# Kernel optimization log

Measured on AMD Instinct MI355X. Metric: run time of the kernel, lower is better.

The kernel has to match this reference:

```python
import jax, jax.numpy as jnp
import numpy as np

N, E, G = 50000, 800000, 64
D, DE, DIN, L = 64, 4, 11, 2


def _lin(x, w, b):
    return x @ w + b


def _bn(x, g, b, eps=1e-5):
    # BatchNorm1d in training mode: biased batch statistics over dim 0
    m = x.mean(0)
    v = x.var(0)
    return (x - m) * jax.lax.rsqrt(v + eps) * g + b


def setup_inputs() -> dict:
    key = jax.random.key(0)
    ks = iter(jax.random.split(key, 64))

    def rn(shape, s=0.05):
        return jax.random.normal(next(ks), shape, jnp.float32) * s

    inp = dict(
        x=rn((N, DIN), 1.0),
        pos=rn((N, 3), 1.0),
        edge_attr=rn((E, DE), 1.0),
        edge_index=jax.random.randint(next(ks), (2, E), 0, N),
        batch=jnp.sort(jax.random.randint(next(ks), (N,), 0, G)),
        lin_in_w=rn((DIN, D)), lin_in_b=jnp.zeros((D,), jnp.float32),
        lin_pred_w=rn((D, 1)), lin_pred_b=jnp.zeros((1,), jnp.float32),
        # per-layer stacked params (leading dim L)
        msg_w1=rn((L, 2 * D + DE + 1, D)), msg_b1=jnp.zeros((L, D), jnp.float32),
        msg_g1=jnp.ones((L, D), jnp.float32), msg_be1=jnp.zeros((L, D), jnp.float32),
        msg_w2=rn((L, D, D)), msg_b2=jnp.zeros((L, D), jnp.float32),
        msg_g2=jnp.ones((L, D), jnp.float32), msg_be2=jnp.zeros((L, D), jnp.float32),
        pos_w1=rn((L, D, D)), pos_b1=jnp.zeros((L, D), jnp.float32),
        pos_g=jnp.ones((L, D), jnp.float32), pos_be=jnp.zeros((L, D), jnp.float32),
        pos_w2=rn((L, D, 1)), pos_b2=jnp.zeros((L, 1), jnp.float32),
        upd_w1=rn((L, 2 * D, D)), upd_b1=jnp.zeros((L, D), jnp.float32),
        upd_g1=jnp.ones((L, D), jnp.float32), upd_be1=jnp.zeros((L, D), jnp.float32),
        upd_w2=rn((L, D, D)), upd_b2=jnp.zeros((L, D), jnp.float32),
        upd_g2=jnp.ones((L, D), jnp.float32), upd_be2=jnp.zeros((L, D), jnp.float32),
    )
    return inp


def reference(x, pos, edge_attr, edge_index, batch,
              lin_in_w, lin_in_b, lin_pred_w, lin_pred_b,
              msg_w1, msg_b1, msg_g1, msg_be1, msg_w2, msg_b2, msg_g2, msg_be2,
              pos_w1, pos_b1, pos_g, pos_be, pos_w2, pos_b2,
              upd_w1, upd_b1, upd_g1, upd_be1, upd_w2, upd_b2, upd_g2, upd_be2):
    src, dst = edge_index[0], edge_index[1]  # h_j = h[src], h_i = h[dst]
    h = x @ lin_in_w + lin_in_b
    p = pos
    deg = jnp.maximum(jax.ops.segment_sum(jnp.ones((E,), h.dtype), dst, N), 1.0)
    for l in range(L):
        h_i, h_j = h[dst], h[src]          # (E, D) gathers
        pd = p[dst] - p[src]               # (E, 3)
        radial = jnp.sum(pd * pd, axis=1, keepdims=True)  # (E, 1)
        m = jnp.concatenate([h_i, h_j, radial, edge_attr], -1)  # (E, 2D+DE+1)
        m = jax.nn.relu(_bn(_lin(m, msg_w1[l], msg_b1[l]), msg_g1[l], msg_be1[l]))
        m = jax.nn.relu(_bn(_lin(m, msg_w2[l], msg_b2[l]), msg_g2[l], msg_be2[l]))
        s = jax.nn.relu(_bn(_lin(m, pos_w1[l], pos_b1[l]), pos_g[l], pos_be[l]))
        s = _lin(s, pos_w2[l], pos_b2[l])  # (E, 1) scalar gate
        pos_upd = pd * s                   # (E, 3)
        m_aggr = jax.ops.segment_sum(m, dst, N)                    # sum aggr
        p_aggr = jax.ops.segment_sum(pos_upd, dst, N) / deg[:, None]  # mean aggr
        u = jnp.concatenate([h, m_aggr], -1)
        u = jax.nn.relu(_bn(_lin(u, upd_w1[l], upd_b1[l]), upd_g1[l], upd_be1[l]))
        u = jax.nn.relu(_bn(_lin(u, upd_w2[l], upd_b2[l]), upd_g2[l], upd_be2[l]))
        h = h + u          # residual on node features (MPNNModel style)
        p = p + p_aggr     # position update from layer
    cnt = jnp.maximum(jax.ops.segment_sum(jnp.ones((N,), h.dtype), batch, G), 1.0)
    h_graph = jax.ops.segment_sum(h, batch, G) / cnt[:, None]  # global_mean_pool
    out = h_graph @ lin_pred_w + lin_pred_b
    return out.reshape(-1)
```

## Files before the change

kernel.cpp:

```cpp
#include <hip/hip_runtime.h>

#define Nn 50000
#define Ee 800000
#define Gg 64
#define Dd 64
#define KIN 133
#define ES 68
#define EPS 1e-5f


__global__ __launch_bounds__(256) void k_lin_in(const float* __restrict__ x,
    const float* __restrict__ W, const float* __restrict__ B, float* __restrict__ h)
{
    __shared__ float Ws[11 * 64];
    __shared__ float Bs[64];
    int t = threadIdx.x;
    for (int i = t; i < 11 * 64; i += 256) Ws[i] = W[i];
    if (t < 64) Bs[t] = B[t];
    __syncthreads();
    int i = blockIdx.x * 256 + t;
    if (i < Nn * 64) {
        int n = i >> 6, c = i & 63;
        float acc = Bs[c];
        #pragma unroll
        for (int k = 0; k < 11; k++) acc += x[n * 11 + k] * Ws[k * 64 + c];
        h[i] = acc;
    }
}

__global__ __launch_bounds__(256) void k_deg(const int* __restrict__ ei, float* __restrict__ deg)
{
    int e = blockIdx.x * 256 + threadIdx.x;
    if (e < Ee) atomicAdd(&deg[ei[Ee + e]], 1.f);
}

__global__ __launch_bounds__(256) void k_cnt(const int* __restrict__ batch, float* __restrict__ cnt)
{
    int n = blockIdx.x * 256 + threadIdx.x;
    if (n < Nn) atomicAdd(&cnt[batch[n]], 1.f);
}


__global__ __launch_bounds__(256) void k_edge_lin1(
    const float* __restrict__ h, const float* __restrict__ p,
    const float* __restrict__ ea, const int* __restrict__ ei,
    const float* __restrict__ W, const float* __restrict__ B,
    float* __restrict__ ybuf, float* __restrict__ stats_out)
{
    __shared__ float Ws[KIN * 64];
    __shared__ float Bs[64];
    __shared__ float in_t[KIN * ES];
    int t = threadIdx.x;
    for (int i = t; i < KIN * 64; i += 256) Ws[i] = W[i];
    if (t < 64) Bs[t] = B[t];
    int tx = t & 15, ty = t >> 4;
    int c = t & 63, eg = t >> 6;
    float ssum[4] = {0, 0, 0, 0}, ssq[4] = {0, 0, 0, 0};
    for (int tile = blockIdx.x; tile < Ee / 64; tile += gridDim.x) {
        int te = tile * 64;
        __syncthreads();
        for (int e = eg; e < 64; e += 4) {
            int sr = ei[te + e], ds = ei[Ee + te + e];
            in_t[c * ES + e]        = h[(size_t)ds * 64 + c];
            in_t[(64 + c) * ES + e] = h[(size_t)sr * 64 + c];
        }
        if (t < 64) {
            int e = t;
            int sr = ei[te + e], ds = ei[Ee + te + e];
            float dx = p[ds * 3 + 0] - p[sr * 3 + 0];
            float dy = p[ds * 3 + 1] - p[sr * 3 + 1];
            float dz = p[ds * 3 + 2] - p[sr * 3 + 2];
            in_t[128 * ES + e] = dx * dx + dy * dy + dz * dz;
            float4 a4 = *(const float4*)&ea[(size_t)(te + e) * 4];
            in_t[129 * ES + e] = a4.x;
            in_t[130 * ES + e] = a4.y;
            in_t[131 * ES + e] = a4.z;
            in_t[132 * ES + e] = a4.w;
        }
        __syncthreads();
        float acc[4][4];
        #pragma unroll
        for (int i = 0; i < 4; i++)
            #pragma unroll
            for (int j = 0; j < 4; j++) acc[i][j] = Bs[4 * ty + j];
        for (int k = 0; k < KIN; k++) {
            float av[4], wv[4];
            *(float4*)av = *(const float4*)&in_t[k * ES + 4 * tx];
            *(float4*)wv = *(const float4*)&Ws[k * 64 + 4 * ty];
            #pragma unroll
            for (int i = 0; i < 4; i++)
                #pragma unroll
                for (int j = 0; j < 4; j++)
                    acc[i][j] += av[i] * wv[j];
        }
        #pragma unroll
        for (int i = 0; i < 4; i++) {
            size_t e = (size_t)te + 4 * tx + i;
            float4 o; o.x = acc[i][0]; o.y = acc[i][1]; o.z = acc[i][2]; o.w = acc[i][3];
            *(float4*)&ybuf[e * 64 + 4 * ty] = o;
            #pragma unroll
            for (int j = 0; j < 4; j++) { ssum[j] += acc[i][j]; ssq[j] += acc[i][j] * acc[i][j]; }
        }
    }
    #pragma unroll
    for (int j = 0; j < 4; j++) {
        float s = ssum[j], q = ssq[j];
        #pragma unroll
        for (int o2 = 1; o2 < 16; o2 <<= 1) { s += __shfl_xor(s, o2); q += __shfl_xor(q, o2); }
        if (tx == 0) {
            atomicAdd(&stats_out[4 * ty + j], s);
            atomicAdd(&stats_out[64 + 4 * ty + j], q);
        }
    }
}


template<int AGGR>
__global__ __launch_bounds__(256) void k_edge_lin64(
    const float* __restrict__ stats_in, const float* __restrict__ gg,
    const float* __restrict__ be,
    const float* __restrict__ W, const float* __restrict__ B,
    const int* __restrict__ ei, float* __restrict__ magg,
    float* __restrict__ ybuf, float* __restrict__ stats_out)
{
    __shared__ float Ws[64 * 64];
    __shared__ float As[64], Cs[64], Bs[64];
    __shared__ float in_t[64 * ES];
    int t = threadIdx.x;
    if (t < 64) {
        float mean = stats_in[t] * (1.f / Ee);
        float var  = stats_in[64 + t] * (1.f / Ee) - mean * mean;
        float a = gg[t] * rsqrtf(var + EPS);
        As[t] = a; Cs[t] = be[t] - mean * a; Bs[t] = B[t];
    }
    for (int i = t; i < 64 * 64; i += 256) Ws[i] = W[i];
    int tx = t & 15, ty = t >> 4;
    int c = t & 63, eg = t >> 6;
    float ssum[4] = {0, 0, 0, 0}, ssq[4] = {0, 0, 0, 0};
    for (int tile = blockIdx.x; tile < Ee / 64; tile += gridDim.x) {
        int te = tile * 64;
        __syncthreads();
        for (int e = eg; e < 64; e += 4) {
            float y = ybuf[(size_t)(te + e) * 64 + c];
            in_t[c * ES + e] = fmaxf(As[c] * y + Cs[c], 0.f);
        }
        __syncthreads();
        float acc[4][4];
        #pragma unroll
        for (int i = 0; i < 4; i++)
            #pragma unroll
            for (int j = 0; j < 4; j++) acc[i][j] = Bs[4 * ty + j];
        for (int k = 0; k < 64; k++) {
            float av[4], wv[4];
            *(float4*)av = *(const float4*)&in_t[k * ES + 4 * tx];
            *(float4*)wv = *(const float4*)&Ws[k * 64 + 4 * ty];
            #pragma unroll
            for (int i = 0; i < 4; i++)
                #pragma unroll
                for (int j = 0; j < 4; j++)
                    acc[i][j] += av[i] * wv[j];
        }
        if (AGGR) {
            for (int e = eg; e < 64; e += 4) {
                int ds = ei[Ee + te + e];
                atomicAdd(&magg[(size_t)ds * 64 + c], in_t[c * ES + e]);
            }
        }
        #pragma unroll
        for (int i = 0; i < 4; i++) {
            size_t e = (size_t)te + 4 * tx + i;
            float4 o; o.x = acc[i][0]; o.y = acc[i][1]; o.z = acc[i][2]; o.w = acc[i][3];
            *(float4*)&ybuf[e * 64 + 4 * ty] = o;
            #pragma unroll
            for (int j = 0; j < 4; j++) { ssum[j] += acc[i][j]; ssq[j] += acc[i][j] * acc[i][j]; }
        }
    }
    #pragma unroll
    for (int j = 0; j < 4; j++) {
        float s = ssum[j], q = ssq[j];
        #pragma unroll
        for (int o2 = 1; o2 < 16; o2 <<= 1) { s += __shfl_xor(s, o2); q += __shfl_xor(q, o2); }
        if (tx == 0) {
            atomicAdd(&stats_out[4 * ty + j], s);
            atomicAdd(&stats_out[64 + 4 * ty + j], q);
        }
    }
}


__global__ __launch_bounds__(256) void k_pos2(
    const float* __restrict__ stats_in, const float* __restrict__ gg, const float* __restrict__ be,
    const float* __restrict__ W2, const float* __restrict__ B2,
    const float* __restrict__ p, const int* __restrict__ ei,
    const float* __restrict__ ybuf, float* __restrict__ pagg)
{
    __shared__ float As[64], Cs[64], Ws[64];
    int t = threadIdx.x;
    if (t < 64) {
        float mean = stats_in[t] * (1.f / Ee);
        float var  = stats_in[64 + t] * (1.f / Ee) - mean * mean;
        float a = gg[t] * rsqrtf(var + EPS);
        As[t] = a; Cs[t] = be[t] - mean * a; Ws[t] = W2[t];
    }
    __syncthreads();
    int e = blockIdx.x * 256 + t;
    if (e >= Ee) return;
    float acc = B2[0];
    const float* row = &ybuf[(size_t)e * 64];
    #pragma unroll
    for (int u = 0; u < 16; u++) {
        float4 y = *(const float4*)&row[4 * u];
        acc += fmaxf(As[4 * u + 0] * y.x + Cs[4 * u + 0], 0.f) * Ws[4 * u + 0]
             + fmaxf(As[4 * u + 1] * y.y + Cs[4 * u + 1], 0.f) * Ws[4 * u + 1]
             + fmaxf(As[4 * u + 2] * y.z + Cs[4 * u + 2], 0.f) * Ws[4 * u + 2]
             + fmaxf(As[4 * u + 3] * y.w + Cs[4 * u + 3], 0.f) * Ws[4 * u + 3];
    }
    int sr = ei[e], ds = ei[Ee + e];
    float dx = p[ds * 3 + 0] - p[sr * 3 + 0];
    float dy = p[ds * 3 + 1] - p[sr * 3 + 1];
    float dz = p[ds * 3 + 2] - p[sr * 3 + 2];
    atomicAdd(&pagg[ds * 3 + 0], dx * acc);
    atomicAdd(&pagg[ds * 3 + 1], dy * acc);
    atomicAdd(&pagg[ds * 3 + 2], dz * acc);
}


__global__ __launch_bounds__(256) void k_node_lin1(
    const float* __restrict__ h, const float* __restrict__ magg,
    const float* __restrict__ W, const float* __restrict__ B,
    float* __restrict__ yn, float* __restrict__ stats_out)
{
    __shared__ float Ws[128 * 64];
    __shared__ float Bs[64];
    __shared__ float in_t[128 * ES];
    int t = threadIdx.x;
    for (int i = t; i < 128 * 64; i += 256) Ws[i] = W[i];
    if (t < 64) Bs[t] = B[t];
    int tx = t & 15, ty = t >> 4, c = t & 63, eg = t >> 6;
    float ssum[4] = {0, 0, 0, 0}, ssq[4] = {0, 0, 0, 0};
    int nT = (Nn + 63) / 64;
    for (int tile = blockIdx.x; tile < nT; tile += gridDim.x) {
        int te = tile * 64;
        __syncthreads();
        for (int e = eg; e < 64; e += 4) {
            int n = te + e;
            bool v = n < Nn;
            in_t[c * ES + e]        = v ? h[(size_t)n * 64 + c]    : 0.f;
            in_t[(64 + c) * ES + e] = v ? magg[(size_t)n * 64 + c] : 0.f;
        }
        __syncthreads();
        float acc[4][4];
        #pragma unroll
        for (int i = 0; i < 4; i++)
            #pragma unroll
            for (int j = 0; j < 4; j++) acc[i][j] = Bs[4 * ty + j];
        for (int k = 0; k < 128; k++) {
            float av[4], wv[4];
            *(float4*)av = *(const float4*)&in_t[k * ES + 4 * tx];
            *(float4*)wv = *(const float4*)&Ws[k * 64 + 4 * ty];
            #pragma unroll
            for (int i = 0; i < 4; i++)
                #pragma unroll
                for (int j = 0; j < 4; j++)
                    acc[i][j] += av[i] * wv[j];
        }
        #pragma unroll
        for (int i = 0; i < 4; i++) {
            int n = te + 4 * tx + i;
            if (n < Nn) {
                float4 o; o.x = acc[i][0]; o.y = acc[i][1]; o.z = acc[i][2]; o.w = acc[i][3];
                *(float4*)&yn[(size_t)n * 64 + 4 * ty] = o;
                #pragma unroll
                for (int j = 0; j < 4; j++) { ssum[j] += acc[i][j]; ssq[j] += acc[i][j] * acc[i][j]; }
            }
        }
    }
    #pragma unroll
    for (int j = 0; j < 4; j++) {
        float s = ssum[j], q = ssq[j];
        #pragma unroll
        for (int o2 = 1; o2 < 16; o2 <<= 1) { s += __shfl_xor(s, o2); q += __shfl_xor(q, o2); }
        if (tx == 0) {
            atomicAdd(&stats_out[4 * ty + j], s);
            atomicAdd(&stats_out[64 + 4 * ty + j], q);
        }
    }
}


__global__ __launch_bounds__(256) void k_node_lin64(
    const float* __restrict__ stats_in, const float* __restrict__ gg, const float* __restrict__ be,
    const float* __restrict__ W, const float* __restrict__ B,
    float* __restrict__ yn, float* __restrict__ stats_out)
{
    __shared__ float Ws[64 * 64];
    __shared__ float As[64], Cs[64], Bs[64];
    __shared__ float in_t[64 * ES];
    int t = threadIdx.x;
    if (t < 64) {
        float mean = stats_in[t] * (1.f / Nn);
        float var  = stats_in[64 + t] * (1.f / Nn) - mean * mean;
        float a = gg[t] * rsqrtf(var + EPS);
        As[t] = a; Cs[t] = be[t] - mean * a; Bs[t] = B[t];
    }
    for (int i = t; i < 64 * 64; i += 256) Ws[i] = W[i];
    int tx = t & 15, ty = t >> 4, c = t & 63, eg = t >> 6;
    float ssum[4] = {0, 0, 0, 0}, ssq[4] = {0, 0, 0, 0};
    int nT = (Nn + 63) / 64;
    for (int tile = blockIdx.x; tile < nT; tile += gridDim.x) {
        int te = tile * 64;
        __syncthreads();
        for (int e = eg; e < 64; e += 4) {
            int n = te + e;
            float y = (n < Nn) ? yn[(size_t)n * 64 + c] : 0.f;
            in_t[c * ES + e] = fmaxf(As[c] * y + Cs[c], 0.f);
        }
        __syncthreads();
        float acc[4][4];
        #pragma unroll
        for (int i = 0; i < 4; i++)
            #pragma unroll
            for (int j = 0; j < 4; j++) acc[i][j] = Bs[4 * ty + j];
        for (int k = 0; k < 64; k++) {
            float av[4], wv[4];
            *(float4*)av = *(const float4*)&in_t[k * ES + 4 * tx];
            *(float4*)wv = *(const float4*)&Ws[k * 64 + 4 * ty];
            #pragma unroll
            for (int i = 0; i < 4; i++)
                #pragma unroll
                for (int j = 0; j < 4; j++)
                    acc[i][j] += av[i] * wv[j];
        }
        #pragma unroll
        for (int i = 0; i < 4; i++) {
            int n = te + 4 * tx + i;
            if (n < Nn) {
                float4 o; o.x = acc[i][0]; o.y = acc[i][1]; o.z = acc[i][2]; o.w = acc[i][3];
                *(float4*)&yn[(size_t)n * 64 + 4 * ty] = o;
                #pragma unroll
                for (int j = 0; j < 4; j++) { ssum[j] += acc[i][j]; ssq[j] += acc[i][j] * acc[i][j]; }
            }
        }
    }
    #pragma unroll
    for (int j = 0; j < 4; j++) {
        float s = ssum[j], q = ssq[j];
        #pragma unroll
        for (int o2 = 1; o2 < 16; o2 <<= 1) { s += __shfl_xor(s, o2); q += __shfl_xor(q, o2); }
        if (tx == 0) {
            atomicAdd(&stats_out[4 * ty + j], s);
            atomicAdd(&stats_out[64 + 4 * ty + j], q);
        }
    }
}


__global__ __launch_bounds__(256) void k_node_update(
    const float* __restrict__ stats_in, const float* __restrict__ gg, const float* __restrict__ be,
    const float* __restrict__ yn, float* __restrict__ h,
    const float* __restrict__ p_in, float* __restrict__ p_out,
    const float* __restrict__ pagg, const float* __restrict__ deg)
{
    int i = blockIdx.x * 256 + threadIdx.x;
    if (i < Nn * 64) {
        int c = i & 63;
        float mean = stats_in[c] * (1.f / Nn);
        float var  = stats_in[64 + c] * (1.f / Nn) - mean * mean;
        float a = gg[c] * rsqrtf(var + EPS);
        float cc = be[c] - mean * a;
        h[i] += fmaxf(a * yn[i] + cc, 0.f);
    }
    if (i < Nn * 3) {
        float dg = fmaxf(deg[i / 3], 1.f);
        p_out[i] = p_in[i] + pagg[i] / dg;
    }
}


__global__ __launch_bounds__(256) void k_pool(const int* __restrict__ batch,
    const float* __restrict__ h, float* __restrict__ pool)
{
    int i = blockIdx.x * 256 + threadIdx.x;
    if (i < Nn * 64) {
        int n = i >> 6, c = i & 63;
        atomicAdd(&pool[(size_t)batch[n] * 64 + c], h[i]);
    }
}

__global__ void k_out(const float* __restrict__ pool, const float* __restrict__ cnt,
    const float* __restrict__ W, const float* __restrict__ B, float* __restrict__ out)
{
    int g = threadIdx.x;
    if (g < 64) {
        float acc = 0.f;
        for (int c = 0; c < 64; c++) acc += pool[g * 64 + c] * W[c];
        out[g] = acc / fmaxf(cnt[g], 1.f) + B[0];
    }
}


extern "C" void kernel_launch(void* const* d_in, const int* in_sizes, int n_in,
                              void* d_out, int out_size, void* d_ws, size_t ws_size,
                              hipStream_t stream)
{
    const float* x        = (const float*)d_in[0];
    const float* pos      = (const float*)d_in[1];
    const float* ea       = (const float*)d_in[2];
    const int*   ei       = (const int*)  d_in[3];
    const int*   batch    = (const int*)  d_in[4];
    const float* lin_in_w = (const float*)d_in[5];
    const float* lin_in_b = (const float*)d_in[6];
    const float* lin_pr_w = (const float*)d_in[7];
    const float* lin_pr_b = (const float*)d_in[8];
    const float* msg_w1   = (const float*)d_in[9];
    const float* msg_b1   = (const float*)d_in[10];
    const float* msg_g1   = (const float*)d_in[11];
    const float* msg_be1  = (const float*)d_in[12];
    const float* msg_w2   = (const float*)d_in[13];
    const float* msg_b2   = (const float*)d_in[14];
    const float* msg_g2   = (const float*)d_in[15];
    const float* msg_be2  = (const float*)d_in[16];
    const float* pos_w1   = (const float*)d_in[17];
    const float* pos_b1   = (const float*)d_in[18];
    const float* pos_g    = (const float*)d_in[19];
    const float* pos_be   = (const float*)d_in[20];
    const float* pos_w2   = (const float*)d_in[21];
    const float* pos_b2   = (const float*)d_in[22];
    const float* upd_w1   = (const float*)d_in[23];
    const float* upd_b1   = (const float*)d_in[24];
    const float* upd_g1   = (const float*)d_in[25];
    const float* upd_be1  = (const float*)d_in[26];
    const float* upd_w2   = (const float*)d_in[27];
    const float* upd_b2   = (const float*)d_in[28];
    const float* upd_g2   = (const float*)d_in[29];
    const float* upd_be2  = (const float*)d_in[30];
    float* out = (float*)d_out;

    float* ws = (float*)d_ws;
    size_t o = 0;
    float* h    = ws + o; o += (size_t)Nn * 64;
    float* ybuf = ws + o; o += (size_t)Ee * 64;
    float* yn   = ws + o; o += (size_t)Nn * 64;
    float* magg = ws + o; o += (size_t)Nn * 64;
    float* pagg = ws + o; o += (size_t)Nn * 3;
    float* pws  = ws + o; o += (size_t)Nn * 3;
    float* stats= ws + o; o += 1280;
    float* pool = ws + o; o += 64 * 64;
    float* cnt  = ws + o; o += 64;
    float* deg  = ws + o; o += Nn;
    if (ws_size < o * sizeof(float)) return;

    hipMemsetAsync(stats, 0, (size_t)(1280 + 64 * 64 + 64 + Nn) * sizeof(float), stream);
    k_lin_in<<<(Nn * 64 + 255) / 256, 256, 0, stream>>>(x, lin_in_w, lin_in_b, h);
    k_deg<<<(Ee + 255) / 256, 256, 0, stream>>>(ei, deg);
    k_cnt<<<(Nn + 255) / 256, 256, 0, stream>>>(batch, cnt);

    for (int l = 0; l < 2; l++) {
        hipMemsetAsync(magg, 0, ((size_t)Nn * 64 + (size_t)Nn * 3) * sizeof(float), stream);
        const float* pc = (l == 0) ? pos : pws;
        float* st = stats + (size_t)l * 5 * 128;
        k_edge_lin1<<<512, 256, 0, stream>>>(h, pc, ea, ei,
            msg_w1 + (size_t)l * KIN * 64, msg_b1 + l * 64, ybuf, st + 0 * 128);
        k_edge_lin64<0><<<1024, 256, 0, stream>>>(st + 0 * 128, msg_g1 + l * 64, msg_be1 + l * 64,
            msg_w2 + (size_t)l * 64 * 64, msg_b2 + l * 64, ei, nullptr, ybuf, st + 1 * 128);
        k_edge_lin64<1><<<1024, 256, 0, stream>>>(st + 1 * 128, msg_g2 + l * 64, msg_be2 + l * 64,
            pos_w1 + (size_t)l * 64 * 64, pos_b1 + l * 64, ei, magg, ybuf, st + 2 * 128);
        k_pos2<<<(Ee + 255) / 256, 256, 0, stream>>>(st + 2 * 128, pos_g + l * 64, pos_be + l * 64,
            pos_w2 + l * 64, pos_b2 + l, pc, ei, ybuf, pagg);
        k_node_lin1<<<782, 256, 0, stream>>>(h, magg,
            upd_w1 + (size_t)l * 128 * 64, upd_b1 + l * 64, yn, st + 3 * 128);
        k_node_lin64<<<782, 256, 0, stream>>>(st + 3 * 128, upd_g1 + l * 64, upd_be1 + l * 64,
            upd_w2 + (size_t)l * 64 * 64, upd_b2 + l * 64, yn, st + 4 * 128);
        k_node_update<<<(Nn * 64 + 255) / 256, 256, 0, stream>>>(st + 4 * 128,
            upd_g2 + l * 64, upd_be2 + l * 64, yn, h, pc, pws, pagg, deg);
    }
    k_pool<<<(Nn * 64 + 255) / 256, 256, 0, stream>>>(batch, h, pool);
    k_out<<<1, 64, 0, stream>>>(pool, cnt, lin_pr_w, lin_pr_b, out);
}
```

Baseline: 2.497 ms.

## Store edge activations feature-major and double-buffer edge tiles via direct global-to-LDS loads

The edge activation buffer switches from edge-major to feature-major layout, so each feature column over the edges is contiguous. The edge MLP kernels now stage tiles into double-buffered LDS with global_load_lds, prefetching the next tile during compute. BatchNorm+ReLU is folded into the GEMM inner loop, and the first edge kernel prefetches gathered node features in registers. This aims to hide gather and load latency and to coalesce loads in the pos2 kernel, at the cost of more LDS use, a new atomic pattern in the aggregation, and async-load ordering that relies on the existing barriers.

```diff
diff --git a/kernel.cpp b/kernel.cpp
--- a/kernel.cpp
+++ b/kernel.cpp
@@ -3,10 +3,23 @@
 #define Nn 50000
 #define Ee 800000
 #define Gg 64
-#define Dd 64
 #define KIN 133
 #define ES 68
 #define EPS 1e-5f
+
+#define AS1 __attribute__((address_space(1)))
+#define AS3 __attribute__((address_space(3)))
+
+__device__ __forceinline__ void load_lds16(const float* g, float* s) {
+    __builtin_amdgcn_global_load_lds((const AS1 void*)g, (AS3 void*)s, 16, 0, 0);
+}
+
+__device__ __forceinline__ void stage_lin(const float* __restrict__ g0, float* l0,
+                                          int t, int nfloats) {
+    int l = t & 63, w = t >> 6;
+    for (int ch = w; ch * 256 < nfloats; ch += 4)
+        load_lds16(g0 + ch * 256 + l * 4, l0 + ch * 256);
+}
 
 
 __global__ __launch_bounds__(256) void k_lin_in(const float* __restrict__ x,
@@ -45,7 +58,7 @@
     const float* __restrict__ h, const float* __restrict__ p,
     const float* __restrict__ ea, const int* __restrict__ ei,
     const float* __restrict__ W, const float* __restrict__ B,
-    float* __restrict__ ybuf, float* __restrict__ stats_out)
+    float* __restrict__ ybT, float* __restrict__ stats_out)
 {
     __shared__ float Ws[KIN * 64];
     __shared__ float Bs[64];
@@ -54,35 +67,82 @@
     for (int i = t; i < KIN * 64; i += 256) Ws[i] = W[i];
     if (t < 64) Bs[t] = B[t];
     int tx = t & 15, ty = t >> 4;
-    int c = t & 63, eg = t >> 6;
+    int cg = t & 15, es = t >> 4;
     float ssum[4] = {0, 0, 0, 0}, ssq[4] = {0, 0, 0, 0};
-    for (int tile = blockIdx.x; tile < Ee / 64; tile += gridDim.x) {
+
+    float4 hi[4], hj[4], eav;
+    float rad = 0.f;
+    int nt = Ee / 64;
+    int tile = blockIdx.x;
+
+    {
         int te = tile * 64;
-        __syncthreads();
-        for (int e = eg; e < 64; e += 4) {
-            int sr = ei[te + e], ds = ei[Ee + te + e];
-            in_t[c * ES + e]        = h[(size_t)ds * 64 + c];
-            in_t[(64 + c) * ES + e] = h[(size_t)sr * 64 + c];
+        #pragma unroll
+        for (int i = 0; i < 4; i++) {
+            int e = te + es * 4 + i;
+            int sr = ei[e], ds = ei[Ee + e];
+            hi[i] = *(const float4*)&h[(size_t)ds * 64 + 4 * cg];
+            hj[i] = *(const float4*)&h[(size_t)sr * 64 + 4 * cg];
         }
         if (t < 64) {
-            int e = t;
-            int sr = ei[te + e], ds = ei[Ee + te + e];
+            int e = te + t;
+            int sr = ei[e], ds = ei[Ee + e];
             float dx = p[ds * 3 + 0] - p[sr * 3 + 0];
             float dy = p[ds * 3 + 1] - p[sr * 3 + 1];
             float dz = p[ds * 3 + 2] - p[sr * 3 + 2];
-            in_t[128 * ES + e] = dx * dx + dy * dy + dz * dz;
-            float4 a4 = *(const float4*)&ea[(size_t)(te + e) * 4];
-            in_t[129 * ES + e] = a4.x;
-            in_t[130 * ES + e] = a4.y;
-            in_t[131 * ES + e] = a4.z;
-            in_t[132 * ES + e] = a4.w;
-        }
-        __syncthreads();
+            rad = dx * dx + dy * dy + dz * dz;
+            eav = *(const float4*)&ea[(size_t)e * 4];
+        }
+    }
+    {
+        #pragma unroll
+        for (int i = 0; i < 4; i++) {
+            float4 v, u;
+            v.x = ((const float*)&hi[0])[i]; v.y = ((const float*)&hi[1])[i];
+            v.z = ((const float*)&hi[2])[i]; v.w = ((const float*)&hi[3])[i];
+            u.x = ((const float*)&hj[0])[i]; u.y = ((const float*)&hj[1])[i];
+            u.z = ((const float*)&hj[2])[i]; u.w = ((const float*)&hj[3])[i];
+            *(float4*)&in_t[(4 * cg + i) * ES + es * 4] = v;
+            *(float4*)&in_t[(64 + 4 * cg + i) * ES + es * 4] = u;
+        }
+        if (t < 64) {
+            in_t[128 * ES + t] = rad;
+            in_t[129 * ES + t] = eav.x; in_t[130 * ES + t] = eav.y;
+            in_t[131 * ES + t] = eav.z; in_t[132 * ES + t] = eav.w;
+        }
+    }
+
+    for (; tile < nt; tile += gridDim.x) {
+        __syncthreads();
+        int nxt = tile + gridDim.x;
+        if (nxt < nt) {
+            int te = nxt * 64;
+            #pragma unroll
+            for (int i = 0; i < 4; i++) {
+                int e = te + es * 4 + i;
+                int sr = ei[e], ds = ei[Ee + e];
+                hi[i] = *(const float4*)&h[(size_t)ds * 64 + 4 * cg];
+                hj[i] = *(const float4*)&h[(size_t)sr * 64 + 4 * cg];
+            }
+            if (t < 64) {
+                int e = te + t;
+                int sr = ei[e], ds = ei[Ee + e];
+                float dx = p[ds * 3 + 0] - p[sr * 3 + 0];
+                float dy = p[ds * 3 + 1] - p[sr * 3 + 1];
+                float dz = p[ds * 3 + 2] - p[sr * 3 + 2];
+                rad = dx * dx + dy * dy + dz * dz;
+                eav = *(const float4*)&ea[(size_t)e * 4];
+            }
+        }
         float acc[4][4];
-        #pragma unroll
-        for (int i = 0; i < 4; i++)
-            #pragma unroll
-            for (int j = 0; j < 4; j++) acc[i][j] = Bs[4 * ty + j];
+        {
+            float4 b4 = *(const float4*)&Bs[4 * ty];
+            #pragma unroll
+            for (int i = 0; i < 4; i++) {
+                acc[i][0] = b4.x; acc[i][1] = b4.y; acc[i][2] = b4.z; acc[i][3] = b4.w;
+            }
+        }
+        #pragma unroll 7
         for (int k = 0; k < KIN; k++) {
             float av[4], wv[4];
             *(float4*)av = *(const float4*)&in_t[k * ES + 4 * tx];
@@ -93,13 +153,31 @@
                 for (int j = 0; j < 4; j++)
                     acc[i][j] += av[i] * wv[j];
         }
-        #pragma unroll
-        for (int i = 0; i < 4; i++) {
-            size_t e = (size_t)te + 4 * tx + i;
-            float4 o; o.x = acc[i][0]; o.y = acc[i][1]; o.z = acc[i][2]; o.w = acc[i][3];
-            *(float4*)&ybuf[e * 64 + 4 * ty] = o;
-            #pragma unroll
-            for (int j = 0; j < 4; j++) { ssum[j] += acc[i][j]; ssq[j] += acc[i][j] * acc[i][j]; }
+        int te = tile * 64;
+        #pragma unroll
+        for (int j = 0; j < 4; j++) {
+            float4 o; o.x = acc[0][j]; o.y = acc[1][j]; o.z = acc[2][j]; o.w = acc[3][j];
+            *(float4*)&ybT[(size_t)(4 * ty + j) * Ee + te + 4 * tx] = o;
+            ssum[j] += o.x + o.y + o.z + o.w;
+            ssq[j]  += o.x * o.x + o.y * o.y + o.z * o.z + o.w * o.w;
+        }
+        __syncthreads();
+        if (nxt < nt) {
+            #pragma unroll
+            for (int i = 0; i < 4; i++) {
+                float4 v, u;
+                v.x = ((const float*)&hi[0])[i]; v.y = ((const float*)&hi[1])[i];
+                v.z = ((const float*)&hi[2])[i]; v.w = ((const float*)&hi[3])[i];
+                u.x = ((const float*)&hj[0])[i]; u.y = ((const float*)&hj[1])[i];
+                u.z = ((const float*)&hj[2])[i]; u.w = ((const float*)&hj[3])[i];
+                *(float4*)&in_t[(4 * cg + i) * ES + es * 4] = v;
+                *(float4*)&in_t[(64 + 4 * cg + i) * ES + es * 4] = u;
+            }
+            if (t < 64) {
+                in_t[128 * ES + t] = rad;
+                in_t[129 * ES + t] = eav.x; in_t[130 * ES + t] = eav.y;
+                in_t[131 * ES + t] = eav.z; in_t[132 * ES + t] = eav.w;
+            }
         }
     }
     #pragma unroll
@@ -121,59 +199,92 @@
     const float* __restrict__ be,
     const float* __restrict__ W, const float* __restrict__ B,
     const int* __restrict__ ei, float* __restrict__ magg,
-    float* __restrict__ ybuf, float* __restrict__ stats_out)
+    float* __restrict__ ybT, float* __restrict__ stats_out)
 {
     __shared__ float Ws[64 * 64];
-    __shared__ float As[64], Cs[64], Bs[64];
-    __shared__ float in_t[64 * ES];
+    __shared__ float in_t[2 * 64 * 64];
+    __shared__ float ACs[128];
+    __shared__ float Bs[64];
     int t = threadIdx.x;
+    int l = t & 63, w = t >> 6;
+    int lr = l >> 4, lc = (l & 15) * 4;
+
+    stage_lin(W, Ws, t, 64 * 64);
     if (t < 64) {
         float mean = stats_in[t] * (1.f / Ee);
         float var  = stats_in[64 + t] * (1.f / Ee) - mean * mean;
         float a = gg[t] * rsqrtf(var + EPS);
-        As[t] = a; Cs[t] = be[t] - mean * a; Bs[t] = B[t];
-    }
-    for (int i = t; i < 64 * 64; i += 256) Ws[i] = W[i];
+        ACs[2 * t] = a; ACs[2 * t + 1] = be[t] - mean * a; Bs[t] = B[t];
+    }
+    int nt = Ee / 64;
+    int tile = blockIdx.x;
+    {
+        int te = tile * 64;
+        #pragma unroll
+        for (int q = 0; q < 4; q++) {
+            int ch = w * 4 + q;
+            load_lds16(ybT + (size_t)(ch * 4 + lr) * Ee + te + lc, in_t + ch * 256);
+        }
+    }
     int tx = t & 15, ty = t >> 4;
-    int c = t & 63, eg = t >> 6;
+    int cur = 0;
     float ssum[4] = {0, 0, 0, 0}, ssq[4] = {0, 0, 0, 0};
-    for (int tile = blockIdx.x; tile < Ee / 64; tile += gridDim.x) {
-        int te = tile * 64;
-        __syncthreads();
-        for (int e = eg; e < 64; e += 4) {
-            float y = ybuf[(size_t)(te + e) * 64 + c];
-            in_t[c * ES + e] = fmaxf(As[c] * y + Cs[c], 0.f);
-        }
-        __syncthreads();
+
+    for (; tile < nt; tile += gridDim.x) {
+        __syncthreads();
+        int nxt = tile + gridDim.x;
+        int dnode = 0;
+        if (AGGR) dnode = ei[Ee + tile * 64 + l];
+        if (nxt < nt) {
+            int te = nxt * 64;
+            float* dst = in_t + (cur ^ 1) * 4096;
+            #pragma unroll
+            for (int q = 0; q < 4; q++) {
+                int ch = w * 4 + q;
+                load_lds16(ybT + (size_t)(ch * 4 + lr) * Ee + te + lc, dst + ch * 256);
+            }
+        }
+        const float* buf = in_t + cur * 4096;
         float acc[4][4];
-        #pragma unroll
-        for (int i = 0; i < 4; i++)
-            #pragma unroll
-            for (int j = 0; j < 4; j++) acc[i][j] = Bs[4 * ty + j];
+        {
+            float4 b4 = *(const float4*)&Bs[4 * ty];
+            #pragma unroll
+            for (int i = 0; i < 4; i++) {
+                acc[i][0] = b4.x; acc[i][1] = b4.y; acc[i][2] = b4.z; acc[i][3] = b4.w;
+            }
+        }
+        #pragma unroll 8
         for (int k = 0; k < 64; k++) {
             float av[4], wv[4];
-            *(float4*)av = *(const float4*)&in_t[k * ES + 4 * tx];
+            *(float4*)av = *(const float4*)&buf[k * 64 + 4 * tx];
             *(float4*)wv = *(const float4*)&Ws[k * 64 + 4 * ty];
+            float a = ACs[2 * k], c = ACs[2 * k + 1];
+            float r[4];
+            #pragma unroll
+            for (int i = 0; i < 4; i++) r[i] = fmaxf(av[i] * a + c, 0.f);
             #pragma unroll
             for (int i = 0; i < 4; i++)
                 #pragma unroll
                 for (int j = 0; j < 4; j++)
-                    acc[i][j] += av[i] * wv[j];
+                    acc[i][j] += r[i] * wv[j];
         }
         if (AGGR) {
-            for (int e = eg; e < 64; e += 4) {
-                int ds = ei[Ee + te + e];
-                atomicAdd(&magg[(size_t)ds * 64 + c], in_t[c * ES + e]);
-            }
-        }
-        #pragma unroll
-        for (int i = 0; i < 4; i++) {
-            size_t e = (size_t)te + 4 * tx + i;
-            float4 o; o.x = acc[i][0]; o.y = acc[i][1]; o.z = acc[i][2]; o.w = acc[i][3];
-            *(float4*)&ybuf[e * 64 + 4 * ty] = o;
-            #pragma unroll
-            for (int j = 0; j < 4; j++) { ssum[j] += acc[i][j]; ssq[j] += acc[i][j] * acc[i][j]; }
-        }
+            #pragma unroll
+            for (int q = 0; q < 16; q++) {
+                int k = w * 16 + q;
+                float v = fmaxf(buf[k * 64 + l] * ACs[2 * k] + ACs[2 * k + 1], 0.f);
+                atomicAdd(&magg[(size_t)dnode * 64 + k], v);
+            }
+        }
+        int te = tile * 64;
+        #pragma unroll
+        for (int j = 0; j < 4; j++) {
+            float4 o; o.x = acc[0][j]; o.y = acc[1][j]; o.z = acc[2][j]; o.w = acc[3][j];
+            *(float4*)&ybT[(size_t)(4 * ty + j) * Ee + te + 4 * tx] = o;
+            ssum[j] += o.x + o.y + o.z + o.w;
+            ssq[j]  += o.x * o.x + o.y * o.y + o.z * o.z + o.w * o.w;
+        }
+        cur ^= 1;
     }
     #pragma unroll
     for (int j = 0; j < 4; j++) {
@@ -192,7 +303,7 @@
     const float* __restrict__ stats_in, const float* __restrict__ gg, const float* __restrict__ be,
     const float* __restrict__ W2, const float* __restrict__ B2,
     const float* __restrict__ p, const int* __restrict__ ei,
-    const float* __restrict__ ybuf, float* __restrict__ pagg)
+    const float* __restrict__ ybT, float* __restrict__ pagg)
 {
     __shared__ float As[64], Cs[64], Ws[64];
     int t = threadIdx.x;
@@ -204,17 +315,10 @@
     }
     __syncthreads();
     int e = blockIdx.x * 256 + t;
-    if (e >= Ee) return;
     float acc = B2[0];
-    const float* row = &ybuf[(size_t)e * 64];
-    #pragma unroll
-    for (int u = 0; u < 16; u++) {
-        float4 y = *(const float4*)&row[4 * u];
-        acc += fmaxf(As[4 * u + 0] * y.x + Cs[4 * u + 0], 0.f) * Ws[4 * u + 0]
-             + fmaxf(As[4 * u + 1] * y.y + Cs[4 * u + 1], 0.f) * Ws[4 * u + 1]
-             + fmaxf(As[4 * u + 2] * y.z + Cs[4 * u + 2], 0.f) * Ws[4 * u + 2]
-             + fmaxf(As[4 * u + 3] * y.w + Cs[4 * u + 3], 0.f) * Ws[4 * u + 3];
-    }
+    #pragma unroll 8
+    for (int k = 0; k < 64; k++)
+        acc += fmaxf(As[k] * ybT[(size_t)k * Ee + e] + Cs[k], 0.f) * Ws[k];
     int sr = ei[e], ds = ei[Ee + e];
     float dx = p[ds * 3 + 0] - p[sr * 3 + 0];
     float dy = p[ds * 3 + 1] - p[sr * 3 + 1];
@@ -439,7 +543,7 @@
     float* ws = (float*)d_ws;
     size_t o = 0;
     float* h    = ws + o; o += (size_t)Nn * 64;
-    float* ybuf = ws + o; o += (size_t)Ee * 64;
+    float* ybT  = ws + o; o += (size_t)Ee * 64;
     float* yn   = ws + o; o += (size_t)Nn * 64;
     float* magg = ws + o; o += (size_t)Nn * 64;
     float* pagg = ws + o; o += (size_t)Nn * 3;
@@ -460,13 +564,13 @@
         const float* pc = (l == 0) ? pos : pws;
         float* st = stats + (size_t)l * 5 * 128;
         k_edge_lin1<<<512, 256, 0, stream>>>(h, pc, ea, ei,
-            msg_w1 + (size_t)l * KIN * 64, msg_b1 + l * 64, ybuf, st + 0 * 128);
-        k_edge_lin64<0><<<1024, 256, 0, stream>>>(st + 0 * 128, msg_g1 + l * 64, msg_be1 + l * 64,
-            msg_w2 + (size_t)l * 64 * 64, msg_b2 + l * 64, ei, nullptr, ybuf, st + 1 * 128);
-        k_edge_lin64<1><<<1024, 256, 0, stream>>>(st + 1 * 128, msg_g2 + l * 64, msg_be2 + l * 64,
-            pos_w1 + (size_t)l * 64 * 64, pos_b1 + l * 64, ei, magg, ybuf, st + 2 * 128);
-        k_pos2<<<(Ee + 255) / 256, 256, 0, stream>>>(st + 2 * 128, pos_g + l * 64, pos_be + l * 64,
-            pos_w2 + l * 64, pos_b2 + l, pc, ei, ybuf, pagg);
+            msg_w1 + (size_t)l * KIN * 64, msg_b1 + l * 64, ybT, st + 0 * 128);
+        k_edge_lin64<0><<<768, 256, 0, stream>>>(st + 0 * 128, msg_g1 + l * 64, msg_be1 + l * 64,
+            msg_w2 + (size_t)l * 64 * 64, msg_b2 + l * 64, ei, nullptr, ybT, st + 1 * 128);
+        k_edge_lin64<1><<<768, 256, 0, stream>>>(st + 1 * 128, msg_g2 + l * 64, msg_be2 + l * 64,
+            pos_w1 + (size_t)l * 64 * 64, pos_b1 + l * 64, ei, magg, ybT, st + 2 * 128);
+        k_pos2<<<Ee / 256, 256, 0, stream>>>(st + 2 * 128, pos_g + l * 64, pos_be + l * 64,
+            pos_w2 + l * 64, pos_b2 + l, pc, ei, ybT, pagg);
         k_node_lin1<<<782, 256, 0, stream>>>(h, magg,
             upd_w1 + (size_t)l * 128 * 64, upd_b1 + l * 64, yn, st + 3 * 128);
         k_node_lin64<<<782, 256, 0, stream>>>(st + 3 * 128, upd_g1 + l * 64, upd_be1 + l * 64,
```

Measured after the change: 7.340 ms. +194.0%, slower.

## Swizzle edge buffers, async LDS loads with double buffering in edge MLP kernels

Applied to the files above, without the earlier changes.

Stores edge activations in an XOR-swizzled row-major layout so tiles can be copied straight into LDS with global_load_lds and read without bank conflicts. The 64-wide edge layers double-buffer the next tile's load behind the current tile's FMA loop and fold BN+ReLU into the operand read. The first edge layer now gathers node rows as float4 and uses k-chunked FMAs. This adds layout coupling across kernels (k_pos2 must unswizzle) and depends on async LDS load ordering being correctly synchronized.

```diff
diff --git a/kernel.cpp b/kernel.cpp
--- a/kernel.cpp
+++ b/kernel.cpp
@@ -2,11 +2,29 @@
 
 #define Nn 50000
 #define Ee 800000
-#define Gg 64
-#define Dd 64
 #define KIN 133
+#define SR 136
 #define ES 68
 #define EPS 1e-5f
+
+#define AS1 __attribute__((address_space(1)))
+#define AS3 __attribute__((address_space(3)))
+
+__device__ __forceinline__ void load_lds16(const float* g, float* s) {
+    __builtin_amdgcn_global_load_lds((const AS1 void*)g, (AS3 void*)s, 16, 0, 0);
+}
+
+#define BNRELU4(V, A4, C4) \
+    V.x = fmaxf(V.x * A4.x + C4.x, 0.f); \
+    V.y = fmaxf(V.y * A4.y + C4.y, 0.f); \
+    V.z = fmaxf(V.z * A4.z + C4.z, 0.f); \
+    V.w = fmaxf(V.w * A4.w + C4.w, 0.f);
+
+#define FMAROW(ACCI, AV) \
+    ACCI[0] += AV.x * w0.x; ACCI[0] += AV.y * w1.x; ACCI[0] += AV.z * w2.x; ACCI[0] += AV.w * w3.x; \
+    ACCI[1] += AV.x * w0.y; ACCI[1] += AV.y * w1.y; ACCI[1] += AV.z * w2.y; ACCI[1] += AV.w * w3.y; \
+    ACCI[2] += AV.x * w0.z; ACCI[2] += AV.y * w1.z; ACCI[2] += AV.z * w2.z; ACCI[2] += AV.w * w3.z; \
+    ACCI[3] += AV.x * w0.w; ACCI[3] += AV.y * w1.w; ACCI[3] += AV.z * w2.w; ACCI[3] += AV.w * w3.w;
 
 
 __global__ __launch_bounds__(256) void k_lin_in(const float* __restrict__ x,
@@ -47,22 +65,36 @@
     const float* __restrict__ W, const float* __restrict__ B,
     float* __restrict__ ybuf, float* __restrict__ stats_out)
 {
-    __shared__ float Ws[KIN * 64];
+    __shared__ float Ws[SR * 64];
     __shared__ float Bs[64];
-    __shared__ float in_t[KIN * ES];
+    __shared__ float in_t[64 * SR];
     int t = threadIdx.x;
-    for (int i = t; i < KIN * 64; i += 256) Ws[i] = W[i];
-    if (t < 64) Bs[t] = B[t];
+    {
+        int l = t & 63, w = t >> 6;
+        for (int ch = w; ch < 33; ch += 4)
+            load_lds16(W + ch * 256 + l * 4, Ws + ch * 256);
+    }
+    if (t < 64) { Ws[8448 + t] = W[8448 + t]; Bs[t] = B[t]; }
+    else        { Ws[8512 + (t - 64)] = 0.f; }
+    for (int i = t; i < 64 * 3; i += 256)
+        in_t[(i / 3) * SR + 133 + (i % 3)] = 0.f;
+
     int tx = t & 15, ty = t >> 4;
-    int c = t & 63, eg = t >> 6;
+    int cg = t & 15, eu = t >> 4;
     float ssum[4] = {0, 0, 0, 0}, ssq[4] = {0, 0, 0, 0};
+
     for (int tile = blockIdx.x; tile < Ee / 64; tile += gridDim.x) {
         int te = tile * 64;
         __syncthreads();
-        for (int e = eg; e < 64; e += 4) {
+        #pragma unroll
+        for (int b = 0; b < 4; b++) {
+            int e = eu + 16 * b;
             int sr = ei[te + e], ds = ei[Ee + te + e];
-            in_t[c * ES + e]        = h[(size_t)ds * 64 + c];
-            in_t[(64 + c) * ES + e] = h[(size_t)sr * 64 + c];
+            float4 vi = *(const float4*)&h[(size_t)ds * 64 + 4 * cg];
+            float4 vj = *(const float4*)&h[(size_t)sr * 64 + 4 * cg];
+            int qp = (cg ^ eu) * 4;
+            *(float4*)&in_t[e * SR + qp] = vi;
+            *(float4*)&in_t[e * SR + 64 + qp] = vj;
         }
         if (t < 64) {
             int e = t;
@@ -70,36 +102,44 @@
             float dx = p[ds * 3 + 0] - p[sr * 3 + 0];
             float dy = p[ds * 3 + 1] - p[sr * 3 + 1];
             float dz = p[ds * 3 + 2] - p[sr * 3 + 2];
-            in_t[128 * ES + e] = dx * dx + dy * dy + dz * dz;
+            in_t[e * SR + 128] = dx * dx + dy * dy + dz * dz;
             float4 a4 = *(const float4*)&ea[(size_t)(te + e) * 4];
-            in_t[129 * ES + e] = a4.x;
-            in_t[130 * ES + e] = a4.y;
-            in_t[131 * ES + e] = a4.z;
-            in_t[132 * ES + e] = a4.w;
-        }
-        __syncthreads();
+            in_t[e * SR + 129] = a4.x; in_t[e * SR + 130] = a4.y;
+            in_t[e * SR + 131] = a4.z; in_t[e * SR + 132] = a4.w;
+        }
+        __syncthreads();
+
         float acc[4][4];
-        #pragma unroll
-        for (int i = 0; i < 4; i++)
-            #pragma unroll
-            for (int j = 0; j < 4; j++) acc[i][j] = Bs[4 * ty + j];
-        for (int k = 0; k < KIN; k++) {
-            float av[4], wv[4];
-            *(float4*)av = *(const float4*)&in_t[k * ES + 4 * tx];
-            *(float4*)wv = *(const float4*)&Ws[k * 64 + 4 * ty];
-            #pragma unroll
-            for (int i = 0; i < 4; i++)
-                #pragma unroll
-                for (int j = 0; j < 4; j++)
-                    acc[i][j] += av[i] * wv[j];
-        }
+        {
+            float4 b4 = *(const float4*)&Bs[4 * ty];
+            #pragma unroll
+            for (int i = 0; i < 4; i++) {
+                acc[i][0] = b4.x; acc[i][1] = b4.y; acc[i][2] = b4.z; acc[i][3] = b4.w;
+            }
+        }
+        #pragma unroll 2
+        for (int kc = 0; kc < 34; kc++) {
+            int p0 = (kc < 16) ? 4 * (kc ^ tx)
+                   : (kc < 32) ? 64 + 4 * ((kc - 16) ^ tx)
+                               : 4 * kc;
+            float4 a0 = *(const float4*)&in_t[(tx     ) * SR + p0];
+            float4 a1 = *(const float4*)&in_t[(tx + 16) * SR + p0];
+            float4 a2 = *(const float4*)&in_t[(tx + 32) * SR + p0];
+            float4 a3 = *(const float4*)&in_t[(tx + 48) * SR + p0];
+            float4 w0 = *(const float4*)&Ws[(4 * kc + 0) * 64 + 4 * ty];
+            float4 w1 = *(const float4*)&Ws[(4 * kc + 1) * 64 + 4 * ty];
+            float4 w2 = *(const float4*)&Ws[(4 * kc + 2) * 64 + 4 * ty];
+            float4 w3 = *(const float4*)&Ws[(4 * kc + 3) * 64 + 4 * ty];
+            FMAROW(acc[0], a0); FMAROW(acc[1], a1);
+            FMAROW(acc[2], a2); FMAROW(acc[3], a3);
+        }
+        int qp = 4 * (ty ^ tx);
         #pragma unroll
         for (int i = 0; i < 4; i++) {
-            size_t e = (size_t)te + 4 * tx + i;
             float4 o; o.x = acc[i][0]; o.y = acc[i][1]; o.z = acc[i][2]; o.w = acc[i][3];
-            *(float4*)&ybuf[e * 64 + 4 * ty] = o;
-            #pragma unroll
-            for (int j = 0; j < 4; j++) { ssum[j] += acc[i][j]; ssq[j] += acc[i][j] * acc[i][j]; }
+            *(float4*)&ybuf[(size_t)(te + tx + 16 * i) * 64 + qp] = o;
+            ssum[0] += o.x; ssum[1] += o.y; ssum[2] += o.z; ssum[3] += o.w;
+            ssq[0] += o.x * o.x; ssq[1] += o.y * o.y; ssq[2] += o.z * o.z; ssq[3] += o.w * o.w;
         }
     }
     #pragma unroll
@@ -125,55 +165,89 @@
 {
     __shared__ float Ws[64 * 64];
     __shared__ float As[64], Cs[64], Bs[64];
-    __shared__ float in_t[64 * ES];
+    __shared__ float in_t[2 * 64 * 64];
     int t = threadIdx.x;
+    int l = t & 63, w = t >> 6;
+    for (int ch = w; ch < 16; ch += 4)
+        load_lds16(W + ch * 256 + l * 4, Ws + ch * 256);
     if (t < 64) {
         float mean = stats_in[t] * (1.f / Ee);
         float var  = stats_in[64 + t] * (1.f / Ee) - mean * mean;
         float a = gg[t] * rsqrtf(var + EPS);
         As[t] = a; Cs[t] = be[t] - mean * a; Bs[t] = B[t];
     }
-    for (int i = t; i < 64 * 64; i += 256) Ws[i] = W[i];
+    int nt = Ee / 64;
+    int tile = blockIdx.x;
+    {
+        const float* src = ybuf + (size_t)tile * 4096;
+        for (int ch = w; ch < 16; ch += 4)
+            load_lds16(src + ch * 256 + l * 4, in_t + ch * 256);
+    }
     int tx = t & 15, ty = t >> 4;
-    int c = t & 63, eg = t >> 6;
+    int cur = 0;
     float ssum[4] = {0, 0, 0, 0}, ssq[4] = {0, 0, 0, 0};
-    for (int tile = blockIdx.x; tile < Ee / 64; tile += gridDim.x) {
+
+    for (; tile < nt; tile += gridDim.x) {
+        __syncthreads();
         int te = tile * 64;
-        __syncthreads();
-        for (int e = eg; e < 64; e += 4) {
-            float y = ybuf[(size_t)(te + e) * 64 + c];
-            in_t[c * ES + e] = fmaxf(As[c] * y + Cs[c], 0.f);
-        }
-        __syncthreads();
+        int nxt = tile + gridDim.x;
+        int dnode = 0;
+        if (AGGR) dnode = ei[Ee + te + l];
+        if (nxt < nt) {
+            const float* src = ybuf + (size_t)nxt * 4096;
+            float* dst = in_t + (cur ^ 1) * 4096;
+            for (int ch = w; ch < 16; ch += 4)
+                load_lds16(src + ch * 256 + l * 4, dst + ch * 256);
+        }
+        const float* buf = in_t + cur * 4096;
         float acc[4][4];
-        #pragma unroll
-        for (int i = 0; i < 4; i++)
-            #pragma unroll
-            for (int j = 0; j < 4; j++) acc[i][j] = Bs[4 * ty + j];
-        for (int k = 0; k < 64; k++) {
-            float av[4], wv[4];
-            *(float4*)av = *(const float4*)&in_t[k * ES + 4 * tx];
-            *(float4*)wv = *(const float4*)&Ws[k * 64 + 4 * ty];
-            #pragma unroll
-            for (int i = 0; i < 4; i++)
-                #pragma unroll
-                for (int j = 0; j < 4; j++)
-                    acc[i][j] += av[i] * wv[j];
+        {
+            float4 b4 = *(const float4*)&Bs[4 * ty];
+            #pragma unroll
+            for (int i = 0; i < 4; i++) {
+                acc[i][0] = b4.x; acc[i][1] = b4.y; acc[i][2] = b4.z; acc[i][3] = b4.w;
+            }
+        }
+        #pragma unroll 4
+        for (int kc = 0; kc < 16; kc++) {
+            int p0 = 4 * (kc ^ tx);
+            float4 a0 = *(const float4*)&buf[(tx     ) * 64 + p0];
+            float4 a1 = *(const float4*)&buf[(tx + 16) * 64 + p0];
+            float4 a2 = *(const float4*)&buf[(tx + 32) * 64 + p0];
+            float4 a3 = *(const float4*)&buf[(tx + 48) * 64 + p0];
+            float4 as4 = *(const float4*)&As[4 * kc];
+            float4 cs4 = *(const float4*)&Cs[4 * kc];
+            BNRELU4(a0, as4, cs4); BNRELU4(a1, as4, cs4);
+            BNRELU4(a2, as4, cs4); BNRELU4(a3, as4, cs4);
+            float4 w0 = *(const float4*)&Ws[(4 * kc + 0) * 64 + 4 * ty];
+            float4 w1 = *(const float4*)&Ws[(4 * kc + 1) * 64 + 4 * ty];
+            float4 w2 = *(const float4*)&Ws[(4 * kc + 2) * 64 + 4 * ty];
+            float4 w3 = *(const float4*)&Ws[(4 * kc + 3) * 64 + 4 * ty];
+            FMAROW(acc[0], a0); FMAROW(acc[1], a1);
+            FMAROW(acc[2], a2); FMAROW(acc[3], a3);
         }
         if (AGGR) {
-            for (int e = eg; e < 64; e += 4) {
-                int ds = ei[Ee + te + e];
-                atomicAdd(&magg[(size_t)ds * 64 + c], in_t[c * ES + e]);
+            #pragma unroll
+            for (int q = 0; q < 4; q++) {
+                int kq = 4 * q + w;
+                float4 v = *(const float4*)&buf[l * 64 + 4 * (kq ^ (l & 15))];
+                float4 as4 = *(const float4*)&As[4 * kq];
+                float4 cs4 = *(const float4*)&Cs[4 * kq];
+                BNRELU4(v, as4, cs4);
+                float* mg = &magg[(size_t)dnode * 64 + 4 * kq];
+                atomicAdd(mg + 0, v.x); atomicAdd(mg + 1, v.y);
+                atomicAdd(mg + 2, v.z); atomicAdd(mg + 3, v.w);
             }
         }
+        int qp = 4 * (ty ^ tx);
         #pragma unroll
         for (int i = 0; i < 4; i++) {
-            size_t e = (size_t)te + 4 * tx + i;
             float4 o; o.x = acc[i][0]; o.y = acc[i][1]; o.z = acc[i][2]; o.w = acc[i][3];
-            *(float4*)&ybuf[e * 64 + 4 * ty] = o;
-            #pragma unroll
-            for (int j = 0; j < 4; j++) { ssum[j] += acc[i][j]; ssq[j] += acc[i][j] * acc[i][j]; }
-        }
+            *(float4*)&ybuf[(size_t)(te + tx + 16 * i) * 64 + qp] = o;
+            ssum[0] += o.x; ssum[1] += o.y; ssum[2] += o.z; ssum[3] += o.w;
+            ssq[0] += o.x * o.x; ssq[1] += o.y * o.y; ssq[2] += o.z * o.z; ssq[3] += o.w * o.w;
+        }
+        cur ^= 1;
     }
     #pragma unroll
     for (int j = 0; j < 4; j++) {
@@ -204,12 +278,12 @@
     }
     __syncthreads();
     int e = blockIdx.x * 256 + t;
-    if (e >= Ee) return;
+    int em = e & 15;
+    const float* row = &ybuf[(size_t)e * 64];
     float acc = B2[0];
-    const float* row = &ybuf[(size_t)e * 64];
-    #pragma unroll
+    #pragma unroll 4
     for (int u = 0; u < 16; u++) {
-        float4 y = *(const float4*)&row[4 * u];
+        float4 y = *(const float4*)&row[4 * (u ^ em)];
         acc += fmaxf(As[4 * u + 0] * y.x + Cs[4 * u + 0], 0.f) * Ws[4 * u + 0]
              + fmaxf(As[4 * u + 1] * y.y + Cs[4 * u + 1], 0.f) * Ws[4 * u + 1]
              + fmaxf(As[4 * u + 2] * y.z + Cs[4 * u + 2], 0.f) * Ws[4 * u + 2]
@@ -461,11 +535,11 @@
         float* st = stats + (size_t)l * 5 * 128;
         k_edge_lin1<<<512, 256, 0, stream>>>(h, pc, ea, ei,
             msg_w1 + (size_t)l * KIN * 64, msg_b1 + l * 64, ybuf, st + 0 * 128);
-        k_edge_lin64<0><<<1024, 256, 0, stream>>>(st + 0 * 128, msg_g1 + l * 64, msg_be1 + l * 64,
+        k_edge_lin64<0><<<768, 256, 0, stream>>>(st + 0 * 128, msg_g1 + l * 64, msg_be1 + l * 64,
             msg_w2 + (size_t)l * 64 * 64, msg_b2 + l * 64, ei, nullptr, ybuf, st + 1 * 128);
-        k_edge_lin64<1><<<1024, 256, 0, stream>>>(st + 1 * 128, msg_g2 + l * 64, msg_be2 + l * 64,
+        k_edge_lin64<1><<<768, 256, 0, stream>>>(st + 1 * 128, msg_g2 + l * 64, msg_be2 + l * 64,
             pos_w1 + (size_t)l * 64 * 64, pos_b1 + l * 64, ei, magg, ybuf, st + 2 * 128);
-        k_pos2<<<(Ee + 255) / 256, 256, 0, stream>>>(st + 2 * 128, pos_g + l * 64, pos_be + l * 64,
+        k_pos2<<<Ee / 256, 256, 0, stream>>>(st + 2 * 128, pos_g + l * 64, pos_be + l * 64,
             pos_w2 + l * 64, pos_b2 + l, pc, ei, ybuf, pagg);
         k_node_lin1<<<782, 256, 0, stream>>>(h, magg,
             upd_w1 + (size_t)l * 128 * 64, upd_b1 + l * 64, yn, st + 3 * 128);
```

New measurement: 7.731 ms. 3.1x slower.
